# Kernel tuning notes

Measured on AMD Instinct MI355X. Metric: run time of the kernel, lower is better.

Reference implementation:

```python
import jax, jax.numpy as jnp
import numpy as np

H, B, C, T, F = 4, 2, 64, 2048, 64   # n_head, batch, in_chan, time, n_freqs
HID = 4                               # hid_chan (per-head Q/K channels)
VD = C // H                           # per-head V channels
EPS = 1e-5


def prelu(x, a):
    return jnp.where(x >= 0, x, a * x)


def ln_cf(x, g, b):
    # LayerNormalization4D: normalize over (channel, freq) axes of (..., C, T, F)
    mu = x.mean(axis=(-3, -1), keepdims=True)
    var = ((x - mu) ** 2).mean(axis=(-3, -1), keepdims=True)
    return (x - mu) / jnp.sqrt(var + EPS) * g + b


def setup_inputs() -> dict:
    key = jax.random.key(0)
    ks = jax.random.split(key, 8)

    def w(k, shape):
        return jax.random.normal(k, shape, jnp.float32) * 0.05

    return {
        "x": jax.random.normal(ks[0], (B, C, T, F), jnp.float32),
        # per-head 1x1-conv Q/K/V projections (stacked over head axis)
        "Wq": w(ks[1], (H, HID, C)), "bq": jnp.zeros((H, HID), jnp.float32),
        "aq": jnp.full((H,), 0.25, jnp.float32),
        "gq": jnp.ones((H, HID, F), jnp.float32), "betq": jnp.zeros((H, HID, F), jnp.float32),
        "Wk": w(ks[2], (H, HID, C)), "bk": jnp.zeros((H, HID), jnp.float32),
        "ak": jnp.full((H,), 0.25, jnp.float32),
        "gk": jnp.ones((H, HID, F), jnp.float32), "betk": jnp.zeros((H, HID, F), jnp.float32),
        "Wv": w(ks[3], (H, VD, C)), "bv": jnp.zeros((H, VD), jnp.float32),
        "av": jnp.full((H,), 0.25, jnp.float32),
        "gv": jnp.ones((H, VD, F), jnp.float32), "betv": jnp.zeros((H, VD, F), jnp.float32),
        # output 1x1-conv projection
        "Wp": w(ks[4], (C, C)), "bp": jnp.zeros((C,), jnp.float32),
        "ap": jnp.full((), 0.25, jnp.float32),
        "gp": jnp.ones((C, F), jnp.float32), "betp": jnp.zeros((C, F), jnp.float32),
    }


def reference(x, Wq, bq, aq, gq, betq, Wk, bk, ak, gk, betk,
              Wv, bv, av, gv, betv, Wp, bp, ap, gp, betp):
    def qkv(W, b, a, g, be):
        # batched per-head 1x1 conv: (H,O,C) x (B,C,T,F) -> (H,B,O,T,F)
        y = jnp.einsum('hoc,bctf->hbotf', W, x) + b[:, None, :, None, None]
        y = prelu(y, a[:, None, None, None, None])
        return ln_cf(y, g[:, None, :, None, :], be[:, None, :, None, :])

    Q = qkv(Wq, bq, aq, gq, betq).reshape(H * B, HID, T, F)
    K = qkv(Wk, bk, ak, gk, betk).reshape(H * B, HID, T, F)
    V = qkv(Wv, bv, av, gv, betv).reshape(H * B, VD, T, F)

    # (HB, C', T, F) -> (HB, T, C'*F)
    Q = Q.transpose(0, 2, 1, 3).reshape(H * B, T, HID * F)
    K = K.transpose(0, 2, 1, 3).reshape(H * B, T, HID * F)
    V = V.transpose(0, 2, 1, 3).reshape(H * B, T, VD * F)

    scale = 1.0 / jnp.sqrt(jnp.asarray(HID * F, jnp.float32))
    attn = jax.nn.softmax(jnp.einsum('bqd,bkd->bqk', Q, K) * scale, axis=-1)  # (HB,T,T)
    O = jnp.einsum('bqk,bkd->bqd', attn, V)                                    # (HB,T,VD*F)

    # (HB,T,VD,F) -> (B, H*VD, T, F) matching torch head-concat order
    O = O.reshape(H * B, T, VD, F).transpose(0, 2, 1, 3)
    O = O.reshape(H, B, VD, T, F).transpose(1, 0, 2, 3, 4).reshape(B, H * VD, T, F)

    y = jnp.einsum('oc,bctf->botf', Wp, O) + bp[None, :, None, None]
    y = prelu(y, ap)
    y = ln_cf(y, gp[:, None, :], betp[:, None, :])
    return y + x
```

## Files before the change

kernel.cpp:

```cpp
#include <hip/hip_runtime.h>

#define EPS_ 1e-5f

typedef float f32x4 __attribute__((ext_vector_type(4)));
typedef short s16x8 __attribute__((ext_vector_type(8)));

static __device__ __forceinline__ short f2bf(float f) {
    unsigned u = __float_as_uint(f);
    unsigned r = (u + 0x7FFFu + ((u >> 16) & 1u)) >> 16;
    return (short)r;
}
static __device__ __forceinline__ float bf2f(short s) {
    return __uint_as_float(((unsigned)(unsigned short)s) << 16);
}

__global__ __launch_bounds__(256) void prep_kernel(
    const float* __restrict__ Wq, const float* __restrict__ Wk,
    const float* __restrict__ Wv, const float* __restrict__ Wp,
    short* __restrict__ Wbf, short* __restrict__ Wpbf)
{
    int i = blockIdx.x * 256 + threadIdx.x;
    if (i < 6144) {
        float v = (i < 1024) ? Wq[i] : (i < 2048 ? Wk[i - 1024] : Wv[i - 2048]);
        Wbf[i] = f2bf(v);
    } else if (i < 6144 + 4096) {
        Wpbf[i - 6144] = f2bf(Wp[i - 6144]);
    }
}

__global__ __launch_bounds__(256) void qkv_kernel(
    const float* __restrict__ x, const short* __restrict__ Wbf,
    const float* __restrict__ bq, const float* __restrict__ aq,
    const float* __restrict__ gq, const float* __restrict__ betq,
    const float* __restrict__ bk, const float* __restrict__ ak,
    const float* __restrict__ gk, const float* __restrict__ betk,
    const float* __restrict__ bv, const float* __restrict__ av,
    const float* __restrict__ gv, const float* __restrict__ betv,
    short* __restrict__ Qo, short* __restrict__ Ko, short* __restrict__ Vo)
{
    const int t = blockIdx.x;
    const int b = blockIdx.y;
    const int tid = threadIdx.x;
    const int wid = tid >> 6, lane = tid & 63;
    const int g = lane >> 4, c16 = lane & 15;
    const int f_ = tid & 63, cg = tid >> 6;

    __shared__ __align__(16) short wlds[96 * 64];
    __shared__ __align__(16) short xs[64 * 64];
    __shared__ float zs[96 * 64];
    __shared__ float stats[12][2];
    __shared__ float bias_l[96], alpha_l[96];

#pragma unroll
    for (int j = 0; j < 3; ++j) {
        int i8 = tid + 256 * j;
        int row = i8 >> 3, cb = i8 & 7;
        s16x8 v = *(const s16x8*)(Wbf + i8 * 8);
        *(s16x8*)&wlds[row * 64 + ((cb ^ (row & 7)) * 8)] = v;
    }
    if (tid < 96) {
        int row = tid; float bias, al;
        if (row < 16)      { bias = bq[row];      al = aq[row >> 2]; }
        else if (row < 32) { bias = bk[row - 16]; al = ak[(row - 16) >> 2]; }
        else               { bias = bv[row - 32]; al = av[(row - 32) >> 4]; }
        bias_l[row] = bias; alpha_l[row] = al;
    }
#pragma unroll
    for (int it = 0; it < 2; ++it) {
        int cb = cg + 4 * it, c0 = cb * 8;
        s16x8 v;
#pragma unroll
        for (int i = 0; i < 8; ++i)
            v[i] = f2bf(x[(((size_t)b * 64 + c0 + i) * 2048 + t) * 64 + f_]);
        *(s16x8*)&xs[f_ * 64 + ((cb ^ (f_ & 7)) * 8)] = v;
    }
    __syncthreads();

    const int f0 = wid * 16;
    s16x8 bfr[2];
#pragma unroll
    for (int kk = 0; kk < 2; ++kk)
        bfr[kk] = *(const s16x8*)&xs[(f0 + c16) * 64 + (((kk * 4 + g) ^ (c16 & 7)) * 8)];

    f32x4 acc[6];
#pragma unroll
    for (int rt = 0; rt < 6; ++rt) {
#pragma unroll
        for (int r = 0; r < 4; ++r) acc[rt][r] = 0.f;
#pragma unroll
        for (int kk = 0; kk < 2; ++kk) {
            s16x8 a = *(const s16x8*)&wlds[(rt * 16 + c16) * 64 + (((kk * 4 + g) ^ (c16 & 7)) * 8)];
            acc[rt] = __builtin_amdgcn_mfma_f32_16x16x32_bf16(a, bfr[kk], acc[rt], 0, 0, 0);
        }
    }

#pragma unroll
    for (int rt = 0; rt < 6; ++rt)
#pragma unroll
        for (int r = 0; r < 4; ++r) {
            int row = rt * 16 + g * 4 + r;
            float z = acc[rt][r] + bias_l[row];
            z = z >= 0.f ? z : alpha_l[row] * z;
            zs[row * 64 + f0 + c16] = z;
        }
    __syncthreads();

#pragma unroll
    for (int gi = 0; gi < 3; ++gi) {
        int grp = wid * 3 + gi;
        int base_row, n;
        if (grp < 4)      { base_row = grp * 4;             n = 256; }
        else if (grp < 8) { base_row = 16 + (grp - 4) * 4;  n = 256; }
        else              { base_row = 32 + (grp - 8) * 16; n = 1024; }
        int cnt = n >> 6;
        float s = 0.f, ss = 0.f;
        for (int i = 0; i < cnt; ++i) {
            float v = zs[(base_row + i) * 64 + lane];
            s += v; ss += v * v;
        }
#pragma unroll
        for (int msk = 32; msk >= 1; msk >>= 1) {
            s  += __shfl_xor(s, msk);
            ss += __shfl_xor(ss, msk);
        }
        if (lane == 0) {
            float mean = s / n;
            float var = ss / n - mean * mean;
            stats[grp][0] = mean;
            stats[grp][1] = rsqrtf(var + EPS_);
        }
    }
    __syncthreads();

#pragma unroll
    for (int j = 0; j < 24; ++j) {
        int row = cg + 4 * j;
        float zv = zs[row * 64 + f_];
        if (row < 16) {
            int grp = row >> 2;
            float val = (zv - stats[grp][0]) * stats[grp][1];
            val = val * gq[row * 64 + f_] + betq[row * 64 + f_];
            int h = row >> 2, o = row & 3;
            Qo[(((size_t)(h * 2 + b)) * 2048 + t) * 256 + o * 64 + f_] = f2bf(val);
        } else if (row < 32) {
            int rr = row - 16, grp = 4 + (rr >> 2);
            float val = (zv - stats[grp][0]) * stats[grp][1];
            val = val * gk[rr * 64 + f_] + betk[rr * 64 + f_];
            int h = rr >> 2, o = rr & 3;
            Ko[(((size_t)(h * 2 + b)) * 2048 + t) * 256 + o * 64 + f_] = f2bf(val);
        } else {
            int rr = row - 32, grp = 8 + (rr >> 4);
            float val = (zv - stats[grp][0]) * stats[grp][1];
            val = val * gv[rr * 64 + f_] + betv[rr * 64 + f_];
            int h = rr >> 4, ov = rr & 15;
            Vo[(((size_t)(h * 2 + b)) * 2048 + t) * 1024 + ov * 64 + f_] = f2bf(val);
        }
    }
}

__global__ __launch_bounds__(256) void vtrans_kernel(
    const short* __restrict__ Vrm, short* __restrict__ Vt)
{
    const int t0 = blockIdx.x * 64;
    const int d0 = blockIdx.y * 64;
    const int hb = blockIdx.z;
    const int tid = threadIdx.x;
    __shared__ __align__(16) short tile[64 * 72];

#pragma unroll
    for (int k = 0; k < 2; ++k) {
        int q = tid + 256 * k;
        int row = q >> 3, slot = q & 7;
        s16x8 v = *(const s16x8*)(Vrm + ((size_t)hb * 2048 + t0 + row) * 1024 + d0 + slot * 8);
        *(s16x8*)&tile[row * 72 + slot * 8] = v;
    }
    __syncthreads();
#pragma unroll
    for (int k = 0; k < 2; ++k) {
        int q = tid + 256 * k;
        int drow = q >> 3, tslot = q & 7;
        s16x8 v;
#pragma unroll
        for (int i = 0; i < 8; ++i)
            v[i] = tile[(tslot * 8 + i) * 72 + drow];
        *(s16x8*)(Vt + ((size_t)hb * 1024 + d0 + drow) * 2048 + t0 + tslot * 8) = v;
    }
}

__global__ __launch_bounds__(512, 2) void attn_kernel(
    const short* __restrict__ Qg, const short* __restrict__ Kg,
    const short* __restrict__ Vt, short* __restrict__ Ob)
{
    const int hb = blockIdx.x;
    const int qt = blockIdx.y;
    const int t0 = qt * 64;
    const int tid = threadIdx.x;
    const int lane = tid & 63;
    const int wid = tid >> 6;
    const int qs = wid >> 1;
    const int kp = wid & 1;
    const int g = lane >> 4, c16 = lane & 15;

    __shared__ __align__(16) short k_lds[2][64 * 256];
    __shared__ __align__(16) short p_lds[64 * 72];
    __shared__ float lpart[2][64];

    const size_t qbase = ((size_t)hb * 2048 + t0 + qs * 16 + c16) * 256;
    s16x8 qf[8];
#pragma unroll
    for (int kf = 0; kf < 8; ++kf)
        qf[kf] = *(const s16x8*)(Qg + qbase + kf * 32 + g * 8);

    f32x4 oacc[32];
#pragma unroll
    for (int i = 0; i < 32; ++i)
#pragma unroll
        for (int r = 0; r < 4; ++r) oacc[i][r] = 0.f;

    float l_r[4] = {0.f, 0.f, 0.f, 0.f};

    const int srow = tid >> 5, sslot = tid & 31;

    {
        s16x8 kreg0[4];
#pragma unroll
        for (int j = 0; j < 4; ++j) {
            int row = srow + 16 * j;
            kreg0[j] = *(const s16x8*)(Kg + ((size_t)hb * 2048 + row) * 256 + sslot * 8);
        }
#pragma unroll
        for (int j = 0; j < 4; ++j) {
            int row = srow + 16 * j;
            *(s16x8*)&k_lds[0][row * 256 + ((sslot ^ (row & 7)) * 8)] = kreg0[j];
        }
    }
    __syncthreads();

    const int dsl = wid * 128;
    const size_t vrow0 = (size_t)hb * 1024 + dsl + c16;

    for (int tile = 0; tile < 32; ++tile) {
        const int cur = tile & 1;
        const int kt0 = tile * 64;

        s16x8 kreg[4];
        if (tile < 31) {
#pragma unroll
            for (int j = 0; j < 4; ++j) {
                int row = srow + 16 * j;
                kreg[j] = *(const s16x8*)(Kg + ((size_t)hb * 2048 + kt0 + 64 + row) * 256 + sslot * 8);
            }
        }

        f32x4 sf[2];
#pragma unroll
        for (int nf = 0; nf < 2; ++nf)
#pragma unroll
            for (int r = 0; r < 4; ++r) sf[nf][r] = 0.f;
#pragma unroll
        for (int kf = 0; kf < 8; ++kf) {
#pragma unroll
            for (int nf = 0; nf < 2; ++nf) {
                int row = kp * 32 + nf * 16 + c16;
                s16x8 kb = *(const s16x8*)&k_lds[cur][row * 256 + (((kf * 4 + g) ^ (c16 & 7)) * 8)];
                sf[nf] = __builtin_amdgcn_mfma_f32_16x16x32_bf16(qf[kf], kb, sf[nf], 0, 0, 0);
            }
        }

        float rs[4] = {0.f, 0.f, 0.f, 0.f};
#pragma unroll
        for (int nf = 0; nf < 2; ++nf)
#pragma unroll
            for (int r = 0; r < 4; ++r) {
                float p = __expf(sf[nf][r] * 0.0625f);
                sf[nf][r] = p;
                rs[r] += p;
            }
#pragma unroll
        for (int msk = 1; msk <= 8; msk <<= 1)
#pragma unroll
            for (int r = 0; r < 4; ++r) rs[r] += __shfl_xor(rs[r], msk);
#pragma unroll
        for (int r = 0; r < 4; ++r) l_r[r] += rs[r];

#pragma unroll
        for (int nf = 0; nf < 2; ++nf)
#pragma unroll
            for (int r = 0; r < 4; ++r)
                p_lds[(qs * 16 + g * 4 + r) * 72 + kp * 32 + nf * 16 + c16] = f2bf(sf[nf][r]);

        __syncthreads();

        s16x8 pa[4][2];
#pragma unroll
        for (int s4 = 0; s4 < 4; ++s4)
#pragma unroll
            for (int ks = 0; ks < 2; ++ks)
                pa[s4][ks] = *(const s16x8*)&p_lds[(s4 * 16 + c16) * 72 + ks * 32 + g * 8];

        s16x8 vf[3][2];
#pragma unroll
        for (int dt = 0; dt < 2; ++dt)
#pragma unroll
            for (int ks = 0; ks < 2; ++ks)
                vf[dt][ks] = *(const s16x8*)(Vt + (vrow0 + dt * 16) * 2048 + kt0 + (ks * 4 + g) * 8);

#pragma unroll
        for (int dt = 0; dt < 8; ++dt) {
            if (dt < 6) {
#pragma unroll
                for (int ks = 0; ks < 2; ++ks)
                    vf[(dt + 2) % 3][ks] = *(const s16x8*)(Vt + (vrow0 + (dt + 2) * 16) * 2048 + kt0 + (ks * 4 + g) * 8);
            }
#pragma unroll
            for (int s4 = 0; s4 < 4; ++s4)
#pragma unroll
                for (int ks = 0; ks < 2; ++ks)
                    oacc[dt * 4 + s4] = __builtin_amdgcn_mfma_f32_16x16x32_bf16(
                        pa[s4][ks], vf[dt % 3][ks], oacc[dt * 4 + s4], 0, 0, 0);
        }

        if (tile < 31) {
#pragma unroll
            for (int j = 0; j < 4; ++j) {
                int row = srow + 16 * j;
                *(s16x8*)&k_lds[cur ^ 1][row * 256 + ((sslot ^ (row & 7)) * 8)] = kreg[j];
            }
        }
        __syncthreads();
    }

    if (c16 == 0) {
#pragma unroll
        for (int r = 0; r < 4; ++r)
            lpart[kp][qs * 16 + g * 4 + r] = l_r[r];
    }
    __syncthreads();

    float li[16];
#pragma unroll
    for (int s4 = 0; s4 < 4; ++s4)
#pragma unroll
        for (int r = 0; r < 4; ++r) {
            int row = s4 * 16 + g * 4 + r;
            li[s4 * 4 + r] = 1.f / (lpart[0][row] + lpart[1][row]);
        }

    const int h = hb >> 1, b = hb & 1;
#pragma unroll
    for (int dt = 0; dt < 8; ++dt) {
        int vcol = dsl + dt * 16 + c16;
        int cout = h * 16 + (vcol >> 6), ff = vcol & 63;
#pragma unroll
        for (int s4 = 0; s4 < 4; ++s4)
#pragma unroll
            for (int r = 0; r < 4; ++r) {
                int trow = t0 + s4 * 16 + g * 4 + r;
                Ob[(((size_t)b * 64 + cout) * 2048 + trow) * 64 + ff] =
                    f2bf(oacc[dt * 4 + s4][r] * li[s4 * 4 + r]);
            }
    }
}

__global__ __launch_bounds__(256) void oproj_kernel(
    const short* __restrict__ Ob, const float* __restrict__ x,
    const short* __restrict__ Wpbf,
    const float* __restrict__ bp, const float* __restrict__ ap,
    const float* __restrict__ gp, const float* __restrict__ betp,
    float* __restrict__ out)
{
    const int t = blockIdx.x;
    const int b = blockIdx.y;
    const int tid = threadIdx.x;
    const int wid = tid >> 6, lane = tid & 63;
    const int g = lane >> 4, c16 = lane & 15;
    const int f_ = tid & 63, cg = tid >> 6;

    __shared__ __align__(16) short wp[64 * 64];
    __shared__ __align__(16) short os[64 * 64];
    __shared__ float zs[64 * 64];
    __shared__ float red[4][2];

#pragma unroll
    for (int j = 0; j < 2; ++j) {
        int i8 = tid + 256 * j;
        int row = i8 >> 3, cb = i8 & 7;
        s16x8 v = *(const s16x8*)(Wpbf + i8 * 8);
        *(s16x8*)&wp[row * 64 + ((cb ^ (row & 7)) * 8)] = v;
    }
#pragma unroll
    for (int it = 0; it < 2; ++it) {
        int cb = cg + 4 * it, c0 = cb * 8;
        s16x8 v;
#pragma unroll
        for (int i = 0; i < 8; ++i)
            v[i] = Ob[(((size_t)b * 64 + c0 + i) * 2048 + t) * 64 + f_];
        *(s16x8*)&os[f_ * 64 + ((cb ^ (f_ & 7)) * 8)] = v;
    }
    __syncthreads();

    const int f0 = wid * 16;
    s16x8 bfr[2];
#pragma unroll
    for (int kk = 0; kk < 2; ++kk)
        bfr[kk] = *(const s16x8*)&os[(f0 + c16) * 64 + (((kk * 4 + g) ^ (c16 & 7)) * 8)];

    const float ap0 = ap[0];
    f32x4 acc[4];
#pragma unroll
    for (int rt = 0; rt < 4; ++rt) {
#pragma unroll
        for (int r = 0; r < 4; ++r) acc[rt][r] = 0.f;
#pragma unroll
        for (int kk = 0; kk < 2; ++kk) {
            s16x8 a = *(const s16x8*)&wp[(rt * 16 + c16) * 64 + (((kk * 4 + g) ^ (c16 & 7)) * 8)];
            acc[rt] = __builtin_amdgcn_mfma_f32_16x16x32_bf16(a, bfr[kk], acc[rt], 0, 0, 0);
        }
    }

#pragma unroll
    for (int rt = 0; rt < 4; ++rt)
#pragma unroll
        for (int r = 0; r < 4; ++r) {
            int row = rt * 16 + g * 4 + r;
            float z = acc[rt][r] + bp[row];
            z = z >= 0.f ? z : ap0 * z;
            zs[row * 64 + f0 + c16] = z;
        }
    __syncthreads();

    float s = 0.f, ss = 0.f;
#pragma unroll
    for (int j = 0; j < 16; ++j) {
        float v = zs[(cg + 4 * j) * 64 + f_];
        s += v; ss += v * v;
    }
#pragma unroll
    for (int msk = 32; msk >= 1; msk >>= 1) {
        s  += __shfl_xor(s, msk);
        ss += __shfl_xor(ss, msk);
    }
    if (lane == 0) { red[wid][0] = s; red[wid][1] = ss; }
    __syncthreads();
    float ts  = red[0][0] + red[1][0] + red[2][0] + red[3][0];
    float tss = red[0][1] + red[1][1] + red[2][1] + red[3][1];
    float mean = ts * (1.f / 4096.f);
    float rstd = rsqrtf(tss * (1.f / 4096.f) - mean * mean + EPS_);

#pragma unroll
    for (int j = 0; j < 16; ++j) {
        int row = cg + 4 * j;
        size_t idx = (((size_t)b * 64 + row) * 2048 + t) * 64 + f_;
        out[idx] = (zs[row * 64 + f_] - mean) * rstd * gp[row * 64 + f_]
                 + betp[row * 64 + f_] + x[idx];
    }
}

extern "C" void kernel_launch(void* const* d_in, const int* in_sizes, int n_in,
                              void* d_out, int out_size, void* d_ws, size_t ws_size,
                              hipStream_t stream)
{
    const float* x    = (const float*)d_in[0];
    const float* Wq   = (const float*)d_in[1];
    const float* bq   = (const float*)d_in[2];
    const float* aq   = (const float*)d_in[3];
    const float* gq   = (const float*)d_in[4];
    const float* betq = (const float*)d_in[5];
    const float* Wk   = (const float*)d_in[6];
    const float* bk   = (const float*)d_in[7];
    const float* ak   = (const float*)d_in[8];
    const float* gk   = (const float*)d_in[9];
    const float* betk = (const float*)d_in[10];
    const float* Wv   = (const float*)d_in[11];
    const float* bv   = (const float*)d_in[12];
    const float* av   = (const float*)d_in[13];
    const float* gv   = (const float*)d_in[14];
    const float* betv = (const float*)d_in[15];
    const float* Wp   = (const float*)d_in[16];
    const float* bp   = (const float*)d_in[17];
    const float* ap   = (const float*)d_in[18];
    const float* gp   = (const float*)d_in[19];
    const float* betp = (const float*)d_in[20];

    short* Qb   = (short*)d_ws;
    short* Kb   = Qb   + (size_t)8 * 2048 * 256;
    short* Vrm  = Kb   + (size_t)8 * 2048 * 256;
    short* Vt   = Vrm  + (size_t)8 * 2048 * 1024;
    short* Obuf = Vt   + (size_t)8 * 2048 * 1024;
    short* Wbf  = Obuf + (size_t)8 * 2048 * 1024;
    short* Wpbf = Wbf  + 96 * 64;

    prep_kernel<<<40, 256, 0, stream>>>(Wq, Wk, Wv, Wp, Wbf, Wpbf);
    qkv_kernel<<<dim3(2048, 2), 256, 0, stream>>>(x, Wbf,
        bq, aq, gq, betq, bk, ak, gk, betk, bv, av, gv, betv, Qb, Kb, Vrm);
    vtrans_kernel<<<dim3(32, 16, 8), 256, 0, stream>>>(Vrm, Vt);
    attn_kernel<<<dim3(8, 32), 512, 0, stream>>>(Qb, Kb, Vt, Obuf);
    oproj_kernel<<<dim3(2048, 2), 256, 0, stream>>>(Obuf, x, Wpbf,
        bp, ap, gp, betp, (float*)d_out);
}
```

Baseline: 287.3 us.

## Halve attention query tile to 32 rows and split keys across four waves

The attention kernel now handles 32 query rows per block instead of 64, doubling the grid to 512 blocks, and splits each 64-key tile across four waves rather than two. The accumulator count per thread halves, and launch bounds move to 4 blocks per CU so more work can be in flight on the 256 CUs. All V fragments for a tile are now loaded up front instead of through a rolling three-slot buffer, and s_setprio brackets the MFMA sections. The cost is that K and V tiles are reloaded twice as often in total, since each block covers fewer query rows, and LDS per block (~70KB) may keep the 4-blocks-per-CU target from being reached.

New measurement: 1.015 ms. 3.53x slower.

```diff
diff --git a/kernel.cpp b/kernel.cpp
--- a/kernel.cpp
+++ b/kernel.cpp
@@ -187,23 +187,23 @@
     }
 }
 
-__global__ __launch_bounds__(512, 2) void attn_kernel(
+__global__ __launch_bounds__(512, 4) void attn_kernel(
     const short* __restrict__ Qg, const short* __restrict__ Kg,
     const short* __restrict__ Vt, short* __restrict__ Ob)
 {
     const int hb = blockIdx.x;
     const int qt = blockIdx.y;
-    const int t0 = qt * 64;
+    const int t0 = qt * 32;
     const int tid = threadIdx.x;
     const int lane = tid & 63;
     const int wid = tid >> 6;
-    const int qs = wid >> 1;
-    const int kp = wid & 1;
+    const int qs = wid & 1;
+    const int kq = wid >> 1;
     const int g = lane >> 4, c16 = lane & 15;
 
     __shared__ __align__(16) short k_lds[2][64 * 256];
-    __shared__ __align__(16) short p_lds[64 * 72];
-    __shared__ float lpart[2][64];
+    __shared__ __align__(16) short p_lds[32 * 72];
+    __shared__ float lpart[4][32];
 
     const size_t qbase = ((size_t)hb * 2048 + t0 + qs * 16 + c16) * 256;
     s16x8 qf[8];
@@ -211,27 +211,27 @@
     for (int kf = 0; kf < 8; ++kf)
         qf[kf] = *(const s16x8*)(Qg + qbase + kf * 32 + g * 8);
 
-    f32x4 oacc[32];
-#pragma unroll
-    for (int i = 0; i < 32; ++i)
+    f32x4 oacc[16];
+#pragma unroll
+    for (int i = 0; i < 16; ++i)
 #pragma unroll
         for (int r = 0; r < 4; ++r) oacc[i][r] = 0.f;
 
     float l_r[4] = {0.f, 0.f, 0.f, 0.f};
-
-    const int srow = tid >> 5, sslot = tid & 31;
 
     {
         s16x8 kreg0[4];
 #pragma unroll
         for (int j = 0; j < 4; ++j) {
-            int row = srow + 16 * j;
-            kreg0[j] = *(const s16x8*)(Kg + ((size_t)hb * 2048 + row) * 256 + sslot * 8);
+            int q_ = tid + 512 * j;
+            int row = q_ >> 5, slot = q_ & 31;
+            kreg0[j] = *(const s16x8*)(Kg + ((size_t)hb * 2048 + row) * 256 + slot * 8);
         }
 #pragma unroll
         for (int j = 0; j < 4; ++j) {
-            int row = srow + 16 * j;
-            *(s16x8*)&k_lds[0][row * 256 + ((sslot ^ (row & 7)) * 8)] = kreg0[j];
+            int q_ = tid + 512 * j;
+            int row = q_ >> 5, slot = q_ & 31;
+            *(s16x8*)&k_lds[0][row * 256 + ((slot ^ (row & 7)) * 8)] = kreg0[j];
         }
     }
     __syncthreads();
@@ -247,35 +247,31 @@
         if (tile < 31) {
 #pragma unroll
             for (int j = 0; j < 4; ++j) {
-                int row = srow + 16 * j;
-                kreg[j] = *(const s16x8*)(Kg + ((size_t)hb * 2048 + kt0 + 64 + row) * 256 + sslot * 8);
+                int q_ = tid + 512 * j;
+                int row = q_ >> 5, slot = q_ & 31;
+                kreg[j] = *(const s16x8*)(Kg + ((size_t)hb * 2048 + kt0 + 64 + row) * 256 + slot * 8);
             }
         }
 
-        f32x4 sf[2];
-#pragma unroll
-        for (int nf = 0; nf < 2; ++nf)
-#pragma unroll
-            for (int r = 0; r < 4; ++r) sf[nf][r] = 0.f;
+        f32x4 sf;
+#pragma unroll
+        for (int r = 0; r < 4; ++r) sf[r] = 0.f;
+        const int krow = kq * 16 + c16;
+        __builtin_amdgcn_s_setprio(1);
 #pragma unroll
         for (int kf = 0; kf < 8; ++kf) {
-#pragma unroll
-            for (int nf = 0; nf < 2; ++nf) {
-                int row = kp * 32 + nf * 16 + c16;
-                s16x8 kb = *(const s16x8*)&k_lds[cur][row * 256 + (((kf * 4 + g) ^ (c16 & 7)) * 8)];
-                sf[nf] = __builtin_amdgcn_mfma_f32_16x16x32_bf16(qf[kf], kb, sf[nf], 0, 0, 0);
-            }
-        }
-
-        float rs[4] = {0.f, 0.f, 0.f, 0.f};
-#pragma unroll
-        for (int nf = 0; nf < 2; ++nf)
-#pragma unroll
-            for (int r = 0; r < 4; ++r) {
-                float p = __expf(sf[nf][r] * 0.0625f);
-                sf[nf][r] = p;
-                rs[r] += p;
-            }
+            s16x8 kb = *(const s16x8*)&k_lds[cur][krow * 256 + (((kf * 4 + g) ^ (krow & 7)) * 8)];
+            sf = __builtin_amdgcn_mfma_f32_16x16x32_bf16(qf[kf], kb, sf, 0, 0, 0);
+        }
+        __builtin_amdgcn_s_setprio(0);
+
+        float rs[4];
+#pragma unroll
+        for (int r = 0; r < 4; ++r) {
+            float p = __expf(sf[r] * 0.0625f);
+            sf[r] = p;
+            rs[r] = p;
+        }
 #pragma unroll
         for (int msk = 1; msk <= 8; msk <<= 1)
 #pragma unroll
@@ -284,48 +280,43 @@
         for (int r = 0; r < 4; ++r) l_r[r] += rs[r];
 
 #pragma unroll
-        for (int nf = 0; nf < 2; ++nf)
-#pragma unroll
-            for (int r = 0; r < 4; ++r)
-                p_lds[(qs * 16 + g * 4 + r) * 72 + kp * 32 + nf * 16 + c16] = f2bf(sf[nf][r]);
+        for (int r = 0; r < 4; ++r)
+            p_lds[(qs * 16 + g * 4 + r) * 72 + kq * 16 + c16] = f2bf(sf[r]);
 
         __syncthreads();
 
-        s16x8 pa[4][2];
-#pragma unroll
-        for (int s4 = 0; s4 < 4; ++s4)
+        s16x8 pa[2][2];
+#pragma unroll
+        for (int s4 = 0; s4 < 2; ++s4)
 #pragma unroll
             for (int ks = 0; ks < 2; ++ks)
                 pa[s4][ks] = *(const s16x8*)&p_lds[(s4 * 16 + c16) * 72 + ks * 32 + g * 8];
 
-        s16x8 vf[3][2];
-#pragma unroll
-        for (int dt = 0; dt < 2; ++dt)
+        s16x8 vf[8][2];
+#pragma unroll
+        for (int dt = 0; dt < 8; ++dt)
 #pragma unroll
             for (int ks = 0; ks < 2; ++ks)
                 vf[dt][ks] = *(const s16x8*)(Vt + (vrow0 + dt * 16) * 2048 + kt0 + (ks * 4 + g) * 8);
 
-#pragma unroll
-        for (int dt = 0; dt < 8; ++dt) {
-            if (dt < 6) {
+        __builtin_amdgcn_s_setprio(1);
+#pragma unroll
+        for (int dt = 0; dt < 8; ++dt)
+#pragma unroll
+            for (int s4 = 0; s4 < 2; ++s4)
 #pragma unroll
                 for (int ks = 0; ks < 2; ++ks)
-                    vf[(dt + 2) % 3][ks] = *(const s16x8*)(Vt + (vrow0 + (dt + 2) * 16) * 2048 + kt0 + (ks * 4 + g) * 8);
+                    oacc[dt * 2 + s4] = __builtin_amdgcn_mfma_f32_16x16x32_bf16(
+                        pa[s4][ks], vf[dt][ks], oacc[dt * 2 + s4], 0, 0, 0);
+        __builtin_amdgcn_s_setprio(0);
+
+        if (tile < 31) {
+#pragma unroll
+            for (int j = 0; j < 4; ++j) {
+                int q_ = tid + 512 * j;
+                int row = q_ >> 5, slot = q_ & 31;
+                *(s16x8*)&k_lds[cur ^ 1][row * 256 + ((slot ^ (row & 7)) * 8)] = kreg[j];
             }
-#pragma unroll
-            for (int s4 = 0; s4 < 4; ++s4)
-#pragma unroll
-                for (int ks = 0; ks < 2; ++ks)
-                    oacc[dt * 4 + s4] = __builtin_amdgcn_mfma_f32_16x16x32_bf16(
-                        pa[s4][ks], vf[dt % 3][ks], oacc[dt * 4 + s4], 0, 0, 0);
-        }
-
-        if (tile < 31) {
-#pragma unroll
-            for (int j = 0; j < 4; ++j) {
-                int row = srow + 16 * j;
-                *(s16x8*)&k_lds[cur ^ 1][row * 256 + ((sslot ^ (row & 7)) * 8)] = kreg[j];
-            }
         }
         __syncthreads();
     }
@@ -333,17 +324,17 @@
     if (c16 == 0) {
 #pragma unroll
         for (int r = 0; r < 4; ++r)
-            lpart[kp][qs * 16 + g * 4 + r] = l_r[r];
-    }
-    __syncthreads();
-
-    float li[16];
-#pragma unroll
-    for (int s4 = 0; s4 < 4; ++s4)
+            lpart[kq][qs * 16 + g * 4 + r] = l_r[r];
+    }
+    __syncthreads();
+
+    float li[8];
+#pragma unroll
+    for (int s4 = 0; s4 < 2; ++s4)
 #pragma unroll
         for (int r = 0; r < 4; ++r) {
             int row = s4 * 16 + g * 4 + r;
-            li[s4 * 4 + r] = 1.f / (lpart[0][row] + lpart[1][row]);
+            li[s4 * 4 + r] = 1.f / (lpart[0][row] + lpart[1][row] + lpart[2][row] + lpart[3][row]);
         }
 
     const int h = hb >> 1, b = hb & 1;
@@ -352,12 +343,12 @@
         int vcol = dsl + dt * 16 + c16;
         int cout = h * 16 + (vcol >> 6), ff = vcol & 63;
 #pragma unroll
-        for (int s4 = 0; s4 < 4; ++s4)
+        for (int s4 = 0; s4 < 2; ++s4)
 #pragma unroll
             for (int r = 0; r < 4; ++r) {
                 int trow = t0 + s4 * 16 + g * 4 + r;
                 Ob[(((size_t)b * 64 + cout) * 2048 + trow) * 64 + ff] =
-                    f2bf(oacc[dt * 4 + s4][r] * li[s4 * 4 + r]);
+                    f2bf(oacc[dt * 2 + s4][r] * li[s4 * 4 + r]);
             }
     }
 }
@@ -494,7 +485,7 @@
     qkv_kernel<<<dim3(2048, 2), 256, 0, stream>>>(x, Wbf,
         bq, aq, gq, betq, bk, ak, gk, betk, bv, av, gv, betv, Qb, Kb, Vrm);
     vtrans_kernel<<<dim3(32, 16, 8), 256, 0, stream>>>(Vrm, Vt);
-    attn_kernel<<<dim3(8, 32), 512, 0, stream>>>(Qb, Kb, Vt, Obuf);
+    attn_kernel<<<dim3(8, 64), 512, 0, stream>>>(Qb, Kb, Vt, Obuf);
     oproj_kernel<<<dim3(2048, 2), 256, 0, stream>>>(Obuf, x, Wpbf,
         bp, ap, gp, betp, (float*)d_out);
 }
```

## Software-pipeline attention: async K loads to LDS, overlap QK^T with PV

Applied to the files above, without the earlier changes.

Restructures the attention loop so the QK^T/softmax phase for the next key tile runs during the current tile's PV accumulation, using double-buffered P in LDS. K tiles are staged two ahead with direct global-to-LDS loads (global_load_lds), which bypass registers, and one barrier per iteration is removed. MFMA sections are wrapped in s_setprio raises. Q fragments are now reloaded from global memory on every tile rather than kept in registers, which lowers register pressure but adds redundant loads. Correctness depends on the async LDS load being visible by the time of the next barrier.

Result: faster. 265.1 us (-7.7%).

```diff
diff --git a/kernel.cpp b/kernel.cpp
--- a/kernel.cpp
+++ b/kernel.cpp
@@ -12,6 +12,12 @@
 }
 static __device__ __forceinline__ float bf2f(short s) {
     return __uint_as_float(((unsigned)(unsigned short)s) << 16);
+}
+
+static __device__ __forceinline__ void gload16(const short* g, short* l) {
+    __builtin_amdgcn_global_load_lds(
+        (const __attribute__((address_space(1))) unsigned int*)g,
+        (__attribute__((address_space(3))) unsigned int*)l, 16, 0, 0);
 }
 
 __global__ __launch_bounds__(256) void prep_kernel(
@@ -202,134 +208,128 @@
     const int g = lane >> 4, c16 = lane & 15;
 
     __shared__ __align__(16) short k_lds[2][64 * 256];
-    __shared__ __align__(16) short p_lds[64 * 72];
+    __shared__ __align__(16) short p_lds[2][64 * 68];
     __shared__ float lpart[2][64];
 
     const size_t qbase = ((size_t)hb * 2048 + t0 + qs * 16 + c16) * 256;
-    s16x8 qf[8];
-#pragma unroll
-    for (int kf = 0; kf < 8; ++kf)
-        qf[kf] = *(const s16x8*)(Qg + qbase + kf * 32 + g * 8);
-
-    f32x4 oacc[32];
-#pragma unroll
-    for (int i = 0; i < 32; ++i)
-#pragma unroll
-        for (int r = 0; r < 4; ++r) oacc[i][r] = 0.f;
-
-    float l_r[4] = {0.f, 0.f, 0.f, 0.f};
-
-    const int srow = tid >> 5, sslot = tid & 31;
-
-    {
-        s16x8 kreg0[4];
-#pragma unroll
-        for (int j = 0; j < 4; ++j) {
-            int row = srow + 16 * j;
-            kreg0[j] = *(const s16x8*)(Kg + ((size_t)hb * 2048 + row) * 256 + sslot * 8);
-        }
-#pragma unroll
-        for (int j = 0; j < 4; ++j) {
-            int row = srow + 16 * j;
-            *(s16x8*)&k_lds[0][row * 256 + ((sslot ^ (row & 7)) * 8)] = kreg0[j];
-        }
-    }
-    __syncthreads();
-
     const int dsl = wid * 128;
     const size_t vrow0 = (size_t)hb * 1024 + dsl + c16;
-
-    for (int tile = 0; tile < 32; ++tile) {
-        const int cur = tile & 1;
-        const int kt0 = tile * 64;
-
-        s16x8 kreg[4];
-        if (tile < 31) {
-#pragma unroll
-            for (int j = 0; j < 4; ++j) {
-                int row = srow + 16 * j;
-                kreg[j] = *(const s16x8*)(Kg + ((size_t)hb * 2048 + kt0 + 64 + row) * 256 + sslot * 8);
-            }
-        }
-
-        f32x4 sf[2];
-#pragma unroll
-        for (int nf = 0; nf < 2; ++nf)
-#pragma unroll
-            for (int r = 0; r < 4; ++r) sf[nf][r] = 0.f;
-#pragma unroll
-        for (int kf = 0; kf < 8; ++kf) {
-#pragma unroll
-            for (int nf = 0; nf < 2; ++nf) {
-                int row = kp * 32 + nf * 16 + c16;
-                s16x8 kb = *(const s16x8*)&k_lds[cur][row * 256 + (((kf * 4 + g) ^ (c16 & 7)) * 8)];
-                sf[nf] = __builtin_amdgcn_mfma_f32_16x16x32_bf16(qf[kf], kb, sf[nf], 0, 0, 0);
-            }
-        }
-
-        float rs[4] = {0.f, 0.f, 0.f, 0.f};
-#pragma unroll
-        for (int nf = 0; nf < 2; ++nf)
-#pragma unroll
-            for (int r = 0; r < 4; ++r) {
-                float p = __expf(sf[nf][r] * 0.0625f);
-                sf[nf][r] = p;
-                rs[r] += p;
-            }
-#pragma unroll
-        for (int msk = 1; msk <= 8; msk <<= 1)
-#pragma unroll
-            for (int r = 0; r < 4; ++r) rs[r] += __shfl_xor(rs[r], msk);
-#pragma unroll
-        for (int r = 0; r < 4; ++r) l_r[r] += rs[r];
-
-#pragma unroll
-        for (int nf = 0; nf < 2; ++nf)
-#pragma unroll
-            for (int r = 0; r < 4; ++r)
-                p_lds[(qs * 16 + g * 4 + r) * 72 + kp * 32 + nf * 16 + c16] = f2bf(sf[nf][r]);
-
-        __syncthreads();
-
-        s16x8 pa[4][2];
-#pragma unroll
-        for (int s4 = 0; s4 < 4; ++s4)
-#pragma unroll
-            for (int ks = 0; ks < 2; ++ks)
-                pa[s4][ks] = *(const s16x8*)&p_lds[(s4 * 16 + c16) * 72 + ks * 32 + g * 8];
-
-        s16x8 vf[3][2];
+    const size_t kgbase = (size_t)hb * 2048 * 256;
+
+    f32x4 oacc[32];
+#pragma unroll
+    for (int i = 0; i < 32; ++i)
+#pragma unroll
+        for (int r = 0; r < 4; ++r) oacc[i][r] = 0.f;
+
+    float l_r[4] = {0.f, 0.f, 0.f, 0.f};
+
+#define STAGE_K(buf, kt) do {                                                  \
+    _Pragma("unroll")                                                          \
+    for (int j_ = 0; j_ < 4; ++j_) {                                           \
+        int c_ = (wid * 4 + j_) * 64 + lane;                                   \
+        int row_ = c_ >> 5, sp_ = c_ & 31;                                     \
+        int slot_ = sp_ ^ (row_ & 7);                                          \
+        gload16(Kg + kgbase + (size_t)((kt) * 64 + row_) * 256 + slot_ * 8,    \
+                &k_lds[buf][(wid * 4 + j_) * 512]);                            \
+    }                                                                          \
+} while (0)
+
+#define QKT_PHASE(nt) do {                                                     \
+    s16x8 qf[8];                                                               \
+    _Pragma("unroll")                                                          \
+    for (int kf = 0; kf < 8; ++kf)                                             \
+        qf[kf] = *(const s16x8*)(Qg + qbase + kf * 32 + g * 8);                \
+    f32x4 sf[2];                                                               \
+    _Pragma("unroll")                                                          \
+    for (int nf = 0; nf < 2; ++nf)                                             \
+        _Pragma("unroll")                                                      \
+        for (int r = 0; r < 4; ++r) sf[nf][r] = 0.f;                           \
+    __builtin_amdgcn_s_setprio(1);                                             \
+    _Pragma("unroll")                                                          \
+    for (int kf = 0; kf < 8; ++kf) {                                           \
+        _Pragma("unroll")                                                      \
+        for (int nf = 0; nf < 2; ++nf) {                                       \
+            int krow = kp * 32 + nf * 16 + c16;                                \
+            s16x8 kb = *(const s16x8*)&k_lds[(nt) & 1]                         \
+                [krow * 256 + (((kf * 4 + g) ^ (krow & 7)) * 8)];              \
+            sf[nf] = __builtin_amdgcn_mfma_f32_16x16x32_bf16(qf[kf], kb, sf[nf], 0, 0, 0); \
+        }                                                                      \
+    }                                                                          \
+    __builtin_amdgcn_s_setprio(0);                                             \
+    float rs[4] = {0.f, 0.f, 0.f, 0.f};                                        \
+    _Pragma("unroll")                                                          \
+    for (int nf = 0; nf < 2; ++nf)                                             \
+        _Pragma("unroll")                                                      \
+        for (int r = 0; r < 4; ++r) {                                          \
+            float p = __expf(sf[nf][r] * 0.0625f);                             \
+            sf[nf][r] = p;                                                     \
+            rs[r] += p;                                                        \
+        }                                                                      \
+    _Pragma("unroll")                                                          \
+    for (int msk = 1; msk <= 8; msk <<= 1)                                     \
+        _Pragma("unroll")                                                      \
+        for (int r = 0; r < 4; ++r) rs[r] += __shfl_xor(rs[r], msk);           \
+    _Pragma("unroll")                                                          \
+    for (int r = 0; r < 4; ++r) l_r[r] += rs[r];                               \
+    _Pragma("unroll")                                                          \
+    for (int nf = 0; nf < 2; ++nf)                                             \
+        _Pragma("unroll")                                                      \
+        for (int r = 0; r < 4; ++r)                                            \
+            p_lds[(nt) & 1][(qs * 16 + g * 4 + r) * 68 + kp * 32 + nf * 16 + c16] \
+                = f2bf(sf[nf][r]);                                             \
+} while (0)
+
+    STAGE_K(0, 0);
+    __syncthreads();
+    STAGE_K(1, 1);
+    QKT_PHASE(0);
+    __syncthreads();
+
+    for (int t = 0; t < 32; ++t) {
+        const int kt0 = t * 64;
+
+        s16x8 vf[2][2];
 #pragma unroll
         for (int dt = 0; dt < 2; ++dt)
 #pragma unroll
             for (int ks = 0; ks < 2; ++ks)
                 vf[dt][ks] = *(const s16x8*)(Vt + (vrow0 + dt * 16) * 2048 + kt0 + (ks * 4 + g) * 8);
 
+        if (t < 30) STAGE_K(t & 1, t + 2);
+        if (t < 31) QKT_PHASE(t + 1);
+
+        s16x8 pa[4][2];
+#pragma unroll
+        for (int s4 = 0; s4 < 4; ++s4)
+#pragma unroll
+            for (int ks = 0; ks < 2; ++ks)
+                pa[s4][ks] = *(const s16x8*)&p_lds[t & 1][(s4 * 16 + c16) * 68 + ks * 32 + g * 8];
+
 #pragma unroll
         for (int dt = 0; dt < 8; ++dt) {
-            if (dt < 6) {
-#pragma unroll
-                for (int ks = 0; ks < 2; ++ks)
-                    vf[(dt + 2) % 3][ks] = *(const s16x8*)(Vt + (vrow0 + (dt + 2) * 16) * 2048 + kt0 + (ks * 4 + g) * 8);
-            }
+            __builtin_amdgcn_s_setprio(1);
 #pragma unroll
             for (int s4 = 0; s4 < 4; ++s4)
 #pragma unroll
                 for (int ks = 0; ks < 2; ++ks)
                     oacc[dt * 4 + s4] = __builtin_amdgcn_mfma_f32_16x16x32_bf16(
-                        pa[s4][ks], vf[dt % 3][ks], oacc[dt * 4 + s4], 0, 0, 0);
-        }
-
-        if (tile < 31) {
-#pragma unroll
-            for (int j = 0; j < 4; ++j) {
-                int row = srow + 16 * j;
-                *(s16x8*)&k_lds[cur ^ 1][row * 256 + ((sslot ^ (row & 7)) * 8)] = kreg[j];
+                        pa[s4][ks], vf[dt & 1][ks], oacc[dt * 4 + s4], 0, 0, 0);
+            __builtin_amdgcn_s_setprio(0);
+            if (dt < 6) {
+#pragma unroll
+                for (int ks = 0; ks < 2; ++ks)
+                    vf[dt & 1][ks] = *(const s16x8*)(Vt + (vrow0 + (dt + 2) * 16) * 2048 + kt0 + (ks * 4 + g) * 8);
             }
         }
-        __syncthreads();
-    }
-
+
+        if (t < 31) __syncthreads();
+    }
+
+#undef STAGE_K
+#undef QKT_PHASE
+
+    __syncthreads();
     if (c16 == 0) {
 #pragma unroll
         for (int r = 0; r < 4; ++r)
```

## Split attention over V-dim halves and stage K via direct global-to-LDS loads

Applied to the files above, without the earlier changes.

Adds a grid z-dimension that splits the V output dimension in half, so each block computes 64 V columns per wave instead of 128, doubling the block count and halving the accumulator registers. K tiles now go straight from global memory into a single LDS buffer with global_load_lds, replacing the register-staged double buffer. MFMA sections get raised wave priority, and the P tile row stride changes. The trade-off is that QK^T scores and softmax are recomputed twice per query tile. The single K buffer also depends on barrier placement to avoid overwriting K before every wave has read it.

After: 280.9 us. 1.02x faster.

```diff
diff --git a/kernel.cpp b/kernel.cpp
--- a/kernel.cpp
+++ b/kernel.cpp
@@ -12,6 +12,12 @@
 }
 static __device__ __forceinline__ float bf2f(short s) {
     return __uint_as_float(((unsigned)(unsigned short)s) << 16);
+}
+
+static __device__ __forceinline__ void gload16(const short* g, short* l) {
+    __builtin_amdgcn_global_load_lds(
+        (const __attribute__((address_space(1))) unsigned int*)g,
+        (__attribute__((address_space(3))) unsigned int*)l, 16, 0, 0);
 }
 
 __global__ __launch_bounds__(256) void prep_kernel(
@@ -193,6 +199,7 @@
 {
     const int hb = blockIdx.x;
     const int qt = blockIdx.y;
+    const int dh = blockIdx.z;
     const int t0 = qt * 64;
     const int tid = threadIdx.x;
     const int lane = tid & 63;
@@ -201,9 +208,13 @@
     const int kp = wid & 1;
     const int g = lane >> 4, c16 = lane & 15;
 
-    __shared__ __align__(16) short k_lds[2][64 * 256];
-    __shared__ __align__(16) short p_lds[64 * 72];
+    __shared__ __align__(16) short k_lds[64 * 256];
+    __shared__ __align__(16) short p_lds[64 * 68];
     __shared__ float lpart[2][64];
+
+    const size_t kgbase = (size_t)hb * 2048 * 256;
+    const int dsl = dh * 512 + wid * 64;
+    const size_t vrow0 = (size_t)hb * 1024 + dsl + c16;
 
     const size_t qbase = ((size_t)hb * 2048 + t0 + qs * 16 + c16) * 256;
     s16x8 qf[8];
@@ -211,61 +222,54 @@
     for (int kf = 0; kf < 8; ++kf)
         qf[kf] = *(const s16x8*)(Qg + qbase + kf * 32 + g * 8);
 
-    f32x4 oacc[32];
-#pragma unroll
-    for (int i = 0; i < 32; ++i)
+    f32x4 oacc[16];
+#pragma unroll
+    for (int i = 0; i < 16; ++i)
 #pragma unroll
         for (int r = 0; r < 4; ++r) oacc[i][r] = 0.f;
 
     float l_r[4] = {0.f, 0.f, 0.f, 0.f};
 
-    const int srow = tid >> 5, sslot = tid & 31;
-
-    {
-        s16x8 kreg0[4];
-#pragma unroll
-        for (int j = 0; j < 4; ++j) {
-            int row = srow + 16 * j;
-            kreg0[j] = *(const s16x8*)(Kg + ((size_t)hb * 2048 + row) * 256 + sslot * 8);
-        }
-#pragma unroll
-        for (int j = 0; j < 4; ++j) {
-            int row = srow + 16 * j;
-            *(s16x8*)&k_lds[0][row * 256 + ((sslot ^ (row & 7)) * 8)] = kreg0[j];
-        }
-    }
-    __syncthreads();
-
-    const int dsl = wid * 128;
-    const size_t vrow0 = (size_t)hb * 1024 + dsl + c16;
-
-    for (int tile = 0; tile < 32; ++tile) {
-        const int cur = tile & 1;
-        const int kt0 = tile * 64;
-
-        s16x8 kreg[4];
-        if (tile < 31) {
-#pragma unroll
-            for (int j = 0; j < 4; ++j) {
-                int row = srow + 16 * j;
-                kreg[j] = *(const s16x8*)(Kg + ((size_t)hb * 2048 + kt0 + 64 + row) * 256 + sslot * 8);
-            }
-        }
+#define STAGE_K(kt) do {                                                       \
+    _Pragma("unroll")                                                          \
+    for (int j_ = 0; j_ < 4; ++j_) {                                           \
+        int c_ = (wid * 4 + j_) * 64 + lane;                                   \
+        int row_ = c_ >> 5, sp_ = c_ & 31;                                     \
+        int slot_ = sp_ ^ (row_ & 7);                                          \
+        gload16(Kg + kgbase + (size_t)((kt) * 64 + row_) * 256 + slot_ * 8,    \
+                &k_lds[(wid * 4 + j_) * 512]);                                 \
+    }                                                                          \
+} while (0)
+
+    STAGE_K(0);
+    __syncthreads();
+
+    for (int t = 0; t < 32; ++t) {
+        const int kt0 = t * 64;
+
+        s16x8 vf[4][2];
+#pragma unroll
+        for (int dt = 0; dt < 4; ++dt)
+#pragma unroll
+            for (int ks = 0; ks < 2; ++ks)
+                vf[dt][ks] = *(const s16x8*)(Vt + (vrow0 + dt * 16) * 2048 + kt0 + (ks * 4 + g) * 8);
 
         f32x4 sf[2];
 #pragma unroll
         for (int nf = 0; nf < 2; ++nf)
 #pragma unroll
             for (int r = 0; r < 4; ++r) sf[nf][r] = 0.f;
+        __builtin_amdgcn_s_setprio(1);
 #pragma unroll
         for (int kf = 0; kf < 8; ++kf) {
 #pragma unroll
             for (int nf = 0; nf < 2; ++nf) {
-                int row = kp * 32 + nf * 16 + c16;
-                s16x8 kb = *(const s16x8*)&k_lds[cur][row * 256 + (((kf * 4 + g) ^ (c16 & 7)) * 8)];
+                int krow = kp * 32 + nf * 16 + c16;
+                s16x8 kb = *(const s16x8*)&k_lds[krow * 256 + (((kf * 4 + g) ^ (krow & 7)) * 8)];
                 sf[nf] = __builtin_amdgcn_mfma_f32_16x16x32_bf16(qf[kf], kb, sf[nf], 0, 0, 0);
             }
         }
+        __builtin_amdgcn_s_setprio(0);
 
         float rs[4] = {0.f, 0.f, 0.f, 0.f};
 #pragma unroll
@@ -287,48 +291,34 @@
         for (int nf = 0; nf < 2; ++nf)
 #pragma unroll
             for (int r = 0; r < 4; ++r)
-                p_lds[(qs * 16 + g * 4 + r) * 72 + kp * 32 + nf * 16 + c16] = f2bf(sf[nf][r]);
+                p_lds[(qs * 16 + g * 4 + r) * 68 + kp * 32 + nf * 16 + c16] = f2bf(sf[nf][r]);
 
         __syncthreads();
 
+        if (t < 31) STAGE_K(t + 1);
+
         s16x8 pa[4][2];
 #pragma unroll
         for (int s4 = 0; s4 < 4; ++s4)
 #pragma unroll
             for (int ks = 0; ks < 2; ++ks)
-                pa[s4][ks] = *(const s16x8*)&p_lds[(s4 * 16 + c16) * 72 + ks * 32 + g * 8];
-
-        s16x8 vf[3][2];
-#pragma unroll
-        for (int dt = 0; dt < 2; ++dt)
-#pragma unroll
-            for (int ks = 0; ks < 2; ++ks)
-                vf[dt][ks] = *(const s16x8*)(Vt + (vrow0 + dt * 16) * 2048 + kt0 + (ks * 4 + g) * 8);
-
-#pragma unroll
-        for (int dt = 0; dt < 8; ++dt) {
-            if (dt < 6) {
-#pragma unroll
-                for (int ks = 0; ks < 2; ++ks)
-                    vf[(dt + 2) % 3][ks] = *(const s16x8*)(Vt + (vrow0 + (dt + 2) * 16) * 2048 + kt0 + (ks * 4 + g) * 8);
-            }
+                pa[s4][ks] = *(const s16x8*)&p_lds[(s4 * 16 + c16) * 68 + ks * 32 + g * 8];
+
+        __builtin_amdgcn_s_setprio(1);
+#pragma unroll
+        for (int dt = 0; dt < 4; ++dt)
 #pragma unroll
             for (int s4 = 0; s4 < 4; ++s4)
 #pragma unroll
                 for (int ks = 0; ks < 2; ++ks)
                     oacc[dt * 4 + s4] = __builtin_amdgcn_mfma_f32_16x16x32_bf16(
-                        pa[s4][ks], vf[dt % 3][ks], oacc[dt * 4 + s4], 0, 0, 0);
-        }
-
-        if (tile < 31) {
-#pragma unroll
-            for (int j = 0; j < 4; ++j) {
-                int row = srow + 16 * j;
-                *(s16x8*)&k_lds[cur ^ 1][row * 256 + ((sslot ^ (row & 7)) * 8)] = kreg[j];
-            }
-        }
+                        pa[s4][ks], vf[dt][ks], oacc[dt * 4 + s4], 0, 0, 0);
+        __builtin_amdgcn_s_setprio(0);
+
         __syncthreads();
     }
+
+#undef STAGE_K
 
     if (c16 == 0) {
 #pragma unroll
@@ -348,7 +338,7 @@
 
     const int h = hb >> 1, b = hb & 1;
 #pragma unroll
-    for (int dt = 0; dt < 8; ++dt) {
+    for (int dt = 0; dt < 4; ++dt) {
         int vcol = dsl + dt * 16 + c16;
         int cout = h * 16 + (vcol >> 6), ff = vcol & 63;
 #pragma unroll
@@ -494,7 +484,7 @@
     qkv_kernel<<<dim3(2048, 2), 256, 0, stream>>>(x, Wbf,
         bq, aq, gq, betq, bk, ak, gk, betk, bv, av, gv, betv, Qb, Kb, Vrm);
     vtrans_kernel<<<dim3(32, 16, 8), 256, 0, stream>>>(Vrm, Vt);
-    attn_kernel<<<dim3(8, 32), 512, 0, stream>>>(Qb, Kb, Vt, Obuf);
+    attn_kernel<<<dim3(8, 32, 2), 512, 0, stream>>>(Qb, Kb, Vt, Obuf);
     oproj_kernel<<<dim3(2048, 2), 256, 0, stream>>>(Obuf, x, Wpbf,
         bp, ap, gp, betp, (float*)d_out);
 }
```
